# Performance work log

Hardware: AMD Instinct MI355X
Metric: run time of the kernel (lower is better)

## Reference

```python
import jax, jax.numpy as jnp
import numpy as np

B, T, D, H, O = 256, 512, 256, 512, 1


def setup_inputs() -> dict:
    key = jax.random.key(0)
    ks = jax.random.split(key, 7)
    s_ih = 1.0 / np.sqrt(H)
    return {
        "x": jax.random.normal(ks[0], (B, T, D), dtype=jnp.float32),
        "W_ih": jax.random.uniform(ks[1], (4 * H, D), jnp.float32, -s_ih, s_ih),
        "W_hh": jax.random.uniform(ks[2], (4 * H, H), jnp.float32, -s_ih, s_ih),
        "b_ih": jax.random.uniform(ks[3], (4 * H,), jnp.float32, -s_ih, s_ih),
        "b_hh": jax.random.uniform(ks[4], (4 * H,), jnp.float32, -s_ih, s_ih),
        "fc_w": jax.random.uniform(ks[5], (O, H), jnp.float32, -s_ih, s_ih),
        "fc_b": jax.random.uniform(ks[6], (O,), jnp.float32, -s_ih, s_ih),
    }


def reference(x, W_ih, W_hh, b_ih, b_hh, fc_w, fc_b):
    # x: [B, T, D]. Faithful to torch.nn.LSTMCell gate order (i, f, g, o).
    b = b_ih + b_hh
    # Precompute all input projections at once: [T, B, 4H]
    x_t = jnp.swapaxes(x, 0, 1)  # [T, B, D]
    x_proj = jnp.einsum("tbd,gd->tbg", x_t, W_ih) + b

    h0 = jnp.zeros((x.shape[0], W_hh.shape[1]), x.dtype)
    c0 = jnp.zeros_like(h0)

    def step(carry, xp):
        h, c = carry
        gates = xp + h @ W_hh.T  # [B, 4H]
        i, f, g, o = jnp.split(gates, 4, axis=-1)
        c_new = jax.nn.sigmoid(f) * c + jax.nn.sigmoid(i) * jnp.tanh(g)
        h_new = jax.nn.sigmoid(o) * jnp.tanh(c_new)
        return (h_new, c_new), None

    (h_last, _), _ = jax.lax.scan(step, (h0, c0), x_proj)
    out = h_last @ fc_w.T + fc_b  # [B, O]
    return jax.nn.sigmoid(out)
```

## Files before the change

### kernel.cpp

```cpp
#include <hip/hip_runtime.h>
#include <hip/hip_bf16.h>

#define BB 256
#define TT 512
#define DD 256
#define HH 512
#define G4H 2048
#define KTOT 768
#define APITCH 1552
#define WPITCH 1552

typedef unsigned short u16;
typedef unsigned int u32;
typedef __attribute__((ext_vector_type(8))) short bf16x8;
typedef __attribute__((ext_vector_type(4))) float f32x4;

__device__ __forceinline__ u16 f2bf(float f) {
  union { float f; unsigned u; } v; v.f = f;
  unsigned r = v.u + 0x7FFFu + ((v.u >> 16) & 1u);
  return (u16)(r >> 16);
}
__device__ __forceinline__ float bf2f(u16 b) {
  union { unsigned u; float f; } v; v.u = ((unsigned)b) << 16;
  return v.f;
}
__device__ __forceinline__ float fsigmoid(float x) { return 1.f / (1.f + __expf(-x)); }
__device__ __forceinline__ float ftanh(float x) { return 1.f - 2.f / (__expf(2.f * x) + 1.f); }

__device__ __forceinline__ bf16x8 ld16_sc(const u16* p) {
  bf16x8 r;
  asm volatile("global_load_dwordx4 %0, %1, off sc0 sc1" : "=v"(r) : "v"(p) : "memory");
  return r;
}
__device__ __forceinline__ void st4_sc(u16* p, u32 v) {
  asm volatile("global_store_dword %0, %1, off sc0 sc1" :: "v"(p), "v"(v) : "memory");
}
__device__ __forceinline__ void waitv0() {
  asm volatile("s_waitcnt vmcnt(0)" ::: "memory");
}

__global__ __launch_bounds__(256) void lstm_init(
    const float* __restrict__ W_ih, const float* __restrict__ W_hh,
    const float* __restrict__ b_ih, const float* __restrict__ b_hh,
    u16* __restrict__ Wc, float* __restrict__ bsum,
    u16* __restrict__ h0, u32* __restrict__ flags)
{
  int idx = blockIdx.x * 256 + threadIdx.x;
  if (idx < G4H * KTOT) {
    int r = idx / KTOT, k = idx - r * KTOT;
    float v = (k < HH) ? W_hh[r * HH + k] : W_ih[r * DD + (k - HH)];
    Wc[idx] = f2bf(v);
  }
  if (idx < G4H) bsum[idx] = b_ih[idx] + b_hh[idx];
  if (idx < BB * HH) h0[idx] = (u16)0;
  if (idx < 256) flags[idx] = 0u;
}

__global__ __launch_bounds__(256) void xconv(const float* __restrict__ x, u16* __restrict__ xbf)
{
  size_t i = ((size_t)blockIdx.x * 256 + threadIdx.x) * 8;
  float4 a = *(const float4*)(x + i);
  float4 b = *(const float4*)(x + i + 4);
  bf16x8 v;
  v[0] = (short)f2bf(a.x); v[1] = (short)f2bf(a.y);
  v[2] = (short)f2bf(a.z); v[3] = (short)f2bf(a.w);
  v[4] = (short)f2bf(b.x); v[5] = (short)f2bf(b.y);
  v[6] = (short)f2bf(b.z); v[7] = (short)f2bf(b.w);
  *(bf16x8*)(xbf + i) = v;
}

__global__ __launch_bounds__(256, 1) void lstm_persist(
    const u16* __restrict__ xbf, const u16* __restrict__ Wc,
    const float* __restrict__ bsum, u16* __restrict__ h_buf,
    u32* flags)
{
  __shared__ __align__(16) unsigned char Alds[32 * APITCH];
  __shared__ __align__(16) unsigned char Wlds[64 * WPITCH];
  __shared__ float g4[4][32][17];

  const int tid  = threadIdx.x;
  const int bg   = blockIdx.x & 7;
  const int sl   = blockIdx.x >> 3;
  const int lane = tid & 63;
  const int wv   = tid >> 6;
  const int lrow = lane & 15;
  const int lkb  = lane >> 4;

  #pragma unroll
  for (int j = 0; j < 24; ++j) {
    int c = tid + j * 256;
    int r = c / 96, col = c - r * 96;
    int q = r >> 4, u = r & 15;
    bf16x8 v = *(const bf16x8*)(Wc + (size_t)(q * HH + sl * 16 + u) * KTOT + col * 8);
    *(bf16x8*)(Wlds + r * WPITCH + col * 16) = v;
  }

  const int pb2 = tid >> 3;
  const int pu2 = (tid & 7) * 2;
  const int hu2 = sl * 16 + pu2;
  const int gb2 = bg * 32 + pb2;
  const float bi0 = bsum[hu2],          bi1 = bsum[hu2 + 1];
  const float bf0 = bsum[HH + hu2],     bf1 = bsum[HH + hu2 + 1];
  const float bg0 = bsum[2 * HH + hu2], bg1 = bsum[2 * HH + hu2 + 1];
  const float bo0 = bsum[3 * HH + hu2], bo1 = bsum[3 * HH + hu2 + 1];
  float c0 = 0.f, c1 = 0.f;
  u32* myflags = flags + bg * 32;

  for (int t = 0; t < TT; ++t) {
    const u16* __restrict__ h_in  = h_buf + (t & 1) * (BB * HH);
    u16* __restrict__ h_out = h_buf + ((t + 1) & 1) * (BB * HH);

    #pragma unroll
    for (int j = 0; j < 4; ++j) {
      int c = tid + j * 256;
      int row = c >> 5, col = c & 31;
      bf16x8 v = *(const bf16x8*)(xbf + ((size_t)(bg * 32 + row) * TT + t) * DD + col * 8);
      *(bf16x8*)(Alds + row * APITCH + 1024 + col * 16) = v;
    }
    if (t > 0 && wv == 0 && lane < 32) {
      while (__hip_atomic_load(&myflags[lane], __ATOMIC_RELAXED, __HIP_MEMORY_SCOPE_AGENT) < (u32)t)
        __builtin_amdgcn_s_sleep(1);
    }
    __syncthreads();

    bf16x8 hv[8];
    #pragma unroll
    for (int j = 0; j < 8; ++j) {
      int c = tid + j * 256;
      int row = c >> 6, col = c & 63;
      hv[j] = ld16_sc(h_in + (size_t)(bg * 32 + row) * HH + col * 8);
    }
    f32x4 acc0 = {0.f, 0.f, 0.f, 0.f};
    f32x4 acc1 = {0.f, 0.f, 0.f, 0.f};
    {
      const unsigned aox = (unsigned)(lrow * APITCH + 1024 + lkb * 16);
      const unsigned wox = (unsigned)((wv * 16 + lrow) * WPITCH + 1024 + lkb * 16);
      #pragma unroll
      for (int kc = 0; kc < 8; ++kc) {
        bf16x8 bfr = *(const bf16x8*)(Wlds + wox + kc * 64);
        bf16x8 a0  = *(const bf16x8*)(Alds + aox + kc * 64);
        bf16x8 a1  = *(const bf16x8*)(Alds + aox + 16u * APITCH + kc * 64);
        acc0 = __builtin_amdgcn_mfma_f32_16x16x32_bf16(a0, bfr, acc0, 0, 0, 0);
        acc1 = __builtin_amdgcn_mfma_f32_16x16x32_bf16(a1, bfr, acc1, 0, 0, 0);
      }
    }
    waitv0();
    __builtin_amdgcn_sched_barrier(0);
    #pragma unroll
    for (int j = 0; j < 8; ++j) {
      int c = tid + j * 256;
      int row = c >> 6, col = c & 63;
      *(bf16x8*)(Alds + row * APITCH + col * 16) = hv[j];
    }
    __syncthreads();

    {
      const unsigned ao = (unsigned)(lrow * APITCH + lkb * 16);
      const unsigned wo = (unsigned)((wv * 16 + lrow) * WPITCH + lkb * 16);
      #pragma unroll
      for (int kc = 0; kc < 16; ++kc) {
        bf16x8 bfr = *(const bf16x8*)(Wlds + wo + kc * 64);
        bf16x8 a0  = *(const bf16x8*)(Alds + ao + kc * 64);
        bf16x8 a1  = *(const bf16x8*)(Alds + ao + 16u * APITCH + kc * 64);
        acc0 = __builtin_amdgcn_mfma_f32_16x16x32_bf16(a0, bfr, acc0, 0, 0, 0);
        acc1 = __builtin_amdgcn_mfma_f32_16x16x32_bf16(a1, bfr, acc1, 0, 0, 0);
      }
    }
    #pragma unroll
    for (int r = 0; r < 4; ++r) {
      g4[wv][lkb * 4 + r][lrow]      = acc0[r];
      g4[wv][16 + lkb * 4 + r][lrow] = acc1[r];
    }
    __syncthreads();

    {
      float gi0 = g4[0][pb2][pu2]     + bi0, gi1 = g4[0][pb2][pu2 + 1] + bi1;
      float gf_0 = g4[1][pb2][pu2]    + bf0, gf_1 = g4[1][pb2][pu2 + 1] + bf1;
      float gg0 = g4[2][pb2][pu2]     + bg0, gg1 = g4[2][pb2][pu2 + 1] + bg1;
      float go0 = g4[3][pb2][pu2]     + bo0, go1 = g4[3][pb2][pu2 + 1] + bo1;
      c0 = fsigmoid(gf_0) * c0 + fsigmoid(gi0) * ftanh(gg0);
      c1 = fsigmoid(gf_1) * c1 + fsigmoid(gi1) * ftanh(gg1);
      u32 ha = (u32)f2bf(fsigmoid(go0) * ftanh(c0));
      u32 hb = (u32)f2bf(fsigmoid(go1) * ftanh(c1));
      st4_sc(h_out + (size_t)gb2 * HH + hu2, ha | (hb << 16));
    }
    waitv0();
    __syncthreads();
    if (tid == 0)
      __hip_atomic_store(&myflags[sl], (u32)(t + 1), __ATOMIC_RELAXED, __HIP_MEMORY_SCOPE_AGENT);
  }
}

__global__ __launch_bounds__(256) void lstm_final(
    const u16* __restrict__ h, const float* __restrict__ fc_w,
    const float* __restrict__ fc_b, float* __restrict__ out)
{
  int b = threadIdx.x;
  float s = 0.f;
  const u16* hp = h + (size_t)b * HH;
  #pragma unroll 8
  for (int k = 0; k < HH; k += 8) {
    bf16x8 v = *(const bf16x8*)(hp + k);
    #pragma unroll
    for (int j = 0; j < 8; ++j) s += bf2f((u16)v[j]) * fc_w[k + j];
  }
  s += fc_b[0];
  out[b] = fsigmoid(s);
}

extern "C" void kernel_launch(void* const* d_in, const int* in_sizes, int n_in,
                              void* d_out, int out_size, void* d_ws, size_t ws_size,
                              hipStream_t stream) {
  (void)in_sizes; (void)n_in; (void)out_size; (void)ws_size;
  const float* x    = (const float*)d_in[0];
  const float* W_ih = (const float*)d_in[1];
  const float* W_hh = (const float*)d_in[2];
  const float* b_ih = (const float*)d_in[3];
  const float* b_hh = (const float*)d_in[4];
  const float* fc_w = (const float*)d_in[5];
  const float* fc_b = (const float*)d_in[6];
  float* out = (float*)d_out;

  char* ws = (char*)d_ws;
  u16*   Wc    = (u16*)(ws);
  float* bsum  = (float*)(ws + 3145728);
  u16*   h_buf = (u16*)(ws + 3153920);
  u32*   flags = (u32*)(ws + 3678208);
  u16*   xbf   = (u16*)(ws + 4194304);

  lstm_init<<<6144, 256, 0, stream>>>(W_ih, W_hh, b_ih, b_hh, Wc, bsum, h_buf, flags);
  xconv<<<16384, 256, 0, stream>>>(x, xbf);
  void* args[] = { (void*)&xbf, (void*)&Wc, (void*)&bsum, (void*)&h_buf, (void*)&flags };
  (void)hipLaunchCooperativeKernel((void*)lstm_persist, dim3(256), dim3(256), args, 0, stream);
  lstm_final<<<1, 256, 0, stream>>>(h_buf, fc_w, fc_b, out);
}
```

Baseline: 1.689 ms.

## Hold LSTM weights in registers and use 32x32 MFMA with swizzled LDS

Each wave of the persistent LSTM kernel now keeps its slice of the combined weight matrix in VGPRs instead of LDS. It uses 32x32x16 MFMA with a split-K arrangement across wave pairs and two accumulators, plus an XOR-swizzled LDS layout for the activation tile. Weight rows are permuted at init to match the new tiling, and x is transposed to [T,B,D] so per-step loads are contiguous. The spin-wait sleep is removed. The aim is to cut per-step LDS traffic and latency on the serial recurrence, at the cost of heavy register pressure and an extra partial-sum reduction through shared memory.

```diff
diff --git a/kernel.cpp b/kernel.cpp
--- a/kernel.cpp
+++ b/kernel.cpp
@@ -7,13 +7,11 @@
 #define HH 512
 #define G4H 2048
 #define KTOT 768
-#define APITCH 1552
-#define WPITCH 1552
 
 typedef unsigned short u16;
 typedef unsigned int u32;
 typedef __attribute__((ext_vector_type(8))) short bf16x8;
-typedef __attribute__((ext_vector_type(4))) float f32x4;
+typedef __attribute__((ext_vector_type(16))) float f32x16;
 
 __device__ __forceinline__ u16 f2bf(float f) {
   union { float f; unsigned u; } v; v.f = f;
@@ -48,7 +46,11 @@
   int idx = blockIdx.x * 256 + threadIdx.x;
   if (idx < G4H * KTOT) {
     int r = idx / KTOT, k = idx - r * KTOT;
-    float v = (k < HH) ? W_hh[r * HH + k] : W_ih[r * DD + (k - HH)];
+    int slp = r >> 6, rem = r & 63;
+    int q = ((rem >> 5) << 1) | ((rem >> 4) & 1);
+    int u = rem & 15;
+    int srow = q * HH + slp * 16 + u;
+    float v = (k < HH) ? W_hh[srow * HH + k] : W_ih[srow * DD + (k - HH)];
     Wc[idx] = f2bf(v);
   }
   if (idx < G4H) bsum[idx] = b_ih[idx] + b_hh[idx];
@@ -56,43 +58,48 @@
   if (idx < 256) flags[idx] = 0u;
 }
 
-__global__ __launch_bounds__(256) void xconv(const float* __restrict__ x, u16* __restrict__ xbf)
-{
-  size_t i = ((size_t)blockIdx.x * 256 + threadIdx.x) * 8;
-  float4 a = *(const float4*)(x + i);
-  float4 b = *(const float4*)(x + i + 4);
+__global__ __launch_bounds__(256) void xconv(const float* __restrict__ x, u16* __restrict__ xbf2)
+{
+  size_t g = (size_t)blockIdx.x * 256 + threadIdx.x;
+  int d8 = (int)(g & 31);
+  int b  = (int)((g >> 5) & 255);
+  int t  = (int)(g >> 13);
+  const float* src = x + ((size_t)b * TT + t) * DD + d8 * 8;
+  float4 a = *(const float4*)(src);
+  float4 c = *(const float4*)(src + 4);
   bf16x8 v;
   v[0] = (short)f2bf(a.x); v[1] = (short)f2bf(a.y);
   v[2] = (short)f2bf(a.z); v[3] = (short)f2bf(a.w);
-  v[4] = (short)f2bf(b.x); v[5] = (short)f2bf(b.y);
-  v[6] = (short)f2bf(b.z); v[7] = (short)f2bf(b.w);
-  *(bf16x8*)(xbf + i) = v;
+  v[4] = (short)f2bf(c.x); v[5] = (short)f2bf(c.y);
+  v[6] = (short)f2bf(c.z); v[7] = (short)f2bf(c.w);
+  *(bf16x8*)(xbf2 + ((size_t)t * BB + b) * DD + d8 * 8) = v;
 }
 
 __global__ __launch_bounds__(256, 1) void lstm_persist(
-    const u16* __restrict__ xbf, const u16* __restrict__ Wc,
+    const u16* __restrict__ xbf2, const u16* __restrict__ Wc,
     const float* __restrict__ bsum, u16* __restrict__ h_buf,
     u32* flags)
 {
-  __shared__ __align__(16) unsigned char Alds[32 * APITCH];
-  __shared__ __align__(16) unsigned char Wlds[64 * WPITCH];
-  __shared__ float g4[4][32][17];
+  __shared__ __align__(16) unsigned char Alds[49152];
+  __shared__ float g4[2][2][32][66];
 
   const int tid  = threadIdx.x;
   const int bg   = blockIdx.x & 7;
   const int sl   = blockIdx.x >> 3;
   const int lane = tid & 63;
   const int wv   = tid >> 6;
-  const int lrow = lane & 15;
-  const int lkb  = lane >> 4;
-
-  #pragma unroll
-  for (int j = 0; j < 24; ++j) {
-    int c = tid + j * 256;
-    int r = c / 96, col = c - r * 96;
-    int q = r >> 4, u = r & 15;
-    bf16x8 v = *(const bf16x8*)(Wc + (size_t)(q * HH + sl * 16 + u) * KTOT + col * 8);
-    *(bf16x8*)(Wlds + r * WPITCH + col * 16) = v;
+  const int nb   = wv & 1;
+  const int kh   = wv >> 1;
+  const int l31  = lane & 31;
+  const int lhi  = lane >> 5;
+
+  bf16x8 wh[16], wx[8];
+  {
+    const u16* wb = Wc + (size_t)(sl * 64 + nb * 32 + l31) * KTOT + lhi * 8;
+    #pragma unroll
+    for (int i = 0; i < 16; ++i) wh[i] = *(const bf16x8*)(wb + kh * 256 + i * 16);
+    #pragma unroll
+    for (int i = 0; i < 8; ++i)  wx[i] = *(const bf16x8*)(wb + 512 + kh * 128 + i * 16);
   }
 
   const int pb2 = tid >> 3;
@@ -112,72 +119,69 @@
 
     #pragma unroll
     for (int j = 0; j < 4; ++j) {
-      int c = tid + j * 256;
-      int row = c >> 5, col = c & 31;
-      bf16x8 v = *(const bf16x8*)(xbf + ((size_t)(bg * 32 + row) * TT + t) * DD + col * 8);
-      *(bf16x8*)(Alds + row * APITCH + 1024 + col * 16) = v;
+      int idx = j * 256 + tid;
+      int row = idx & 31, d8 = idx >> 5;
+      bf16x8 v = *(const bf16x8*)(xbf2 + ((size_t)t * BB + bg * 32 + row) * DD + d8 * 8);
+      int kc = 32 + (d8 >> 1);
+      int slot = (((d8 & 1) << 5) | row) ^ ((kc & 15) << 2);
+      *(bf16x8*)(Alds + kc * 1024 + slot * 16) = v;
     }
     if (t > 0 && wv == 0 && lane < 32) {
-      while (__hip_atomic_load(&myflags[lane], __ATOMIC_RELAXED, __HIP_MEMORY_SCOPE_AGENT) < (u32)t)
-        __builtin_amdgcn_s_sleep(1);
+      while (__hip_atomic_load(&myflags[lane], __ATOMIC_RELAXED, __HIP_MEMORY_SCOPE_AGENT) < (u32)t) {}
     }
     __syncthreads();
 
     bf16x8 hv[8];
     #pragma unroll
     for (int j = 0; j < 8; ++j) {
-      int c = tid + j * 256;
-      int row = c >> 6, col = c & 63;
-      hv[j] = ld16_sc(h_in + (size_t)(bg * 32 + row) * HH + col * 8);
-    }
-    f32x4 acc0 = {0.f, 0.f, 0.f, 0.f};
-    f32x4 acc1 = {0.f, 0.f, 0.f, 0.f};
-    {
-      const unsigned aox = (unsigned)(lrow * APITCH + 1024 + lkb * 16);
-      const unsigned wox = (unsigned)((wv * 16 + lrow) * WPITCH + 1024 + lkb * 16);
-      #pragma unroll
-      for (int kc = 0; kc < 8; ++kc) {
-        bf16x8 bfr = *(const bf16x8*)(Wlds + wox + kc * 64);
-        bf16x8 a0  = *(const bf16x8*)(Alds + aox + kc * 64);
-        bf16x8 a1  = *(const bf16x8*)(Alds + aox + 16u * APITCH + kc * 64);
-        acc0 = __builtin_amdgcn_mfma_f32_16x16x32_bf16(a0, bfr, acc0, 0, 0, 0);
-        acc1 = __builtin_amdgcn_mfma_f32_16x16x32_bf16(a1, bfr, acc1, 0, 0, 0);
-      }
+      int idx = j * 256 + tid;
+      int row = idx & 31, col8 = idx >> 5;
+      hv[j] = ld16_sc(h_in + (size_t)(bg * 32 + row) * HH + col8 * 8);
+    }
+    f32x16 accA = {0,0,0,0,0,0,0,0,0,0,0,0,0,0,0,0};
+    f32x16 accB = {0,0,0,0,0,0,0,0,0,0,0,0,0,0,0,0};
+    #pragma unroll
+    for (int i = 0; i < 8; ++i) {
+      int kc = 32 + kh * 8 + i;
+      bf16x8 a = *(const bf16x8*)(Alds + kc * 1024 + (size_t)((lane ^ ((kc & 15) << 2)) * 16));
+      if (i & 1) accB = __builtin_amdgcn_mfma_f32_32x32x16_bf16(a, wx[i], accB, 0, 0, 0);
+      else       accA = __builtin_amdgcn_mfma_f32_32x32x16_bf16(a, wx[i], accA, 0, 0, 0);
     }
     waitv0();
     __builtin_amdgcn_sched_barrier(0);
     #pragma unroll
     for (int j = 0; j < 8; ++j) {
-      int c = tid + j * 256;
-      int row = c >> 6, col = c & 63;
-      *(bf16x8*)(Alds + row * APITCH + col * 16) = hv[j];
+      int idx = j * 256 + tid;
+      int row = idx & 31, col8 = idx >> 5;
+      int kc = col8 >> 1;
+      int slot = (((col8 & 1) << 5) | row) ^ ((kc & 15) << 2);
+      *(bf16x8*)(Alds + kc * 1024 + slot * 16) = hv[j];
+    }
+    __syncthreads();
+
+    #pragma unroll
+    for (int i = 0; i < 16; ++i) {
+      int kc = kh * 16 + i;
+      bf16x8 a = *(const bf16x8*)(Alds + kc * 1024 + (size_t)((lane ^ ((kc & 15) << 2)) * 16));
+      if (i & 1) accB = __builtin_amdgcn_mfma_f32_32x32x16_bf16(a, wh[i], accB, 0, 0, 0);
+      else       accA = __builtin_amdgcn_mfma_f32_32x32x16_bf16(a, wh[i], accA, 0, 0, 0);
+    }
+    #pragma unroll
+    for (int r = 0; r < 16; ++r) {
+      int grow = (r & 3) + 8 * (r >> 2) + 4 * lhi;
+      g4[kh][nb][grow][l31] = accA[r] + accB[r];
     }
     __syncthreads();
 
     {
-      const unsigned ao = (unsigned)(lrow * APITCH + lkb * 16);
-      const unsigned wo = (unsigned)((wv * 16 + lrow) * WPITCH + lkb * 16);
-      #pragma unroll
-      for (int kc = 0; kc < 16; ++kc) {
-        bf16x8 bfr = *(const bf16x8*)(Wlds + wo + kc * 64);
-        bf16x8 a0  = *(const bf16x8*)(Alds + ao + kc * 64);
-        bf16x8 a1  = *(const bf16x8*)(Alds + ao + 16u * APITCH + kc * 64);
-        acc0 = __builtin_amdgcn_mfma_f32_16x16x32_bf16(a0, bfr, acc0, 0, 0, 0);
-        acc1 = __builtin_amdgcn_mfma_f32_16x16x32_bf16(a1, bfr, acc1, 0, 0, 0);
-      }
-    }
-    #pragma unroll
-    for (int r = 0; r < 4; ++r) {
-      g4[wv][lkb * 4 + r][lrow]      = acc0[r];
-      g4[wv][16 + lkb * 4 + r][lrow] = acc1[r];
-    }
-    __syncthreads();
-
-    {
-      float gi0 = g4[0][pb2][pu2]     + bi0, gi1 = g4[0][pb2][pu2 + 1] + bi1;
-      float gf_0 = g4[1][pb2][pu2]    + bf0, gf_1 = g4[1][pb2][pu2 + 1] + bf1;
-      float gg0 = g4[2][pb2][pu2]     + bg0, gg1 = g4[2][pb2][pu2 + 1] + bg1;
-      float go0 = g4[3][pb2][pu2]     + bo0, go1 = g4[3][pb2][pu2 + 1] + bo1;
+      float gi0 = g4[0][0][pb2][pu2]      + g4[1][0][pb2][pu2]      + bi0;
+      float gf_0 = g4[0][0][pb2][16 + pu2] + g4[1][0][pb2][16 + pu2] + bf0;
+      float gg0 = g4[0][1][pb2][pu2]      + g4[1][1][pb2][pu2]      + bg0;
+      float go0 = g4[0][1][pb2][16 + pu2] + g4[1][1][pb2][16 + pu2] + bo0;
+      float gi1 = g4[0][0][pb2][pu2 + 1]      + g4[1][0][pb2][pu2 + 1]      + bi1;
+      float gf_1 = g4[0][0][pb2][17 + pu2] + g4[1][0][pb2][17 + pu2] + bf1;
+      float gg1 = g4[0][1][pb2][pu2 + 1]      + g4[1][1][pb2][pu2 + 1]      + bg1;
+      float go1 = g4[0][1][pb2][17 + pu2] + g4[1][1][pb2][17 + pu2] + bo1;
       c0 = fsigmoid(gf_0) * c0 + fsigmoid(gi0) * ftanh(gg0);
       c1 = fsigmoid(gf_1) * c1 + fsigmoid(gi1) * ftanh(gg1);
       u32 ha = (u32)f2bf(fsigmoid(go0) * ftanh(c0));
@@ -226,11 +230,11 @@
   float* bsum  = (float*)(ws + 3145728);
   u16*   h_buf = (u16*)(ws + 3153920);
   u32*   flags = (u32*)(ws + 3678208);
-  u16*   xbf   = (u16*)(ws + 4194304);
+  u16*   xbf2  = (u16*)(ws + 4194304);
 
   lstm_init<<<6144, 256, 0, stream>>>(W_ih, W_hh, b_ih, b_hh, Wc, bsum, h_buf, flags);
-  xconv<<<16384, 256, 0, stream>>>(x, xbf);
-  void* args[] = { (void*)&xbf, (void*)&Wc, (void*)&bsum, (void*)&h_buf, (void*)&flags };
+  xconv<<<16384, 256, 0, stream>>>(x, xbf2);
+  void* args[] = { (void*)&xbf2, (void*)&Wc, (void*)&bsum, (void*)&h_buf, (void*)&flags };
   (void)hipLaunchCooperativeKernel((void*)lstm_persist, dim3(256), dim3(256), args, 0, stream);
   lstm_final<<<1, 256, 0, stream>>>(h_buf, fc_w, fc_b, out);
 }
```

New measurement: 2.078 ms. 1.23x slower.

## Prefetch next-step x tile during current step and store x time-major

Applied to the files above, without the earlier changes.

The input conversion kernel now writes x in [T, B, D] order so each step's tile is contiguous. The persistent LSTM kernel loads the x tile for step t+1 into LDS at the end of step t, before the barrier and the flag wait, overlapping that latency with synchronization. The h-load index mapping is also reshuffled to be row-fastest. Correctness relies on the x LDS region being consumed before the prefetch write.

```diff
diff --git a/kernel.cpp b/kernel.cpp
--- a/kernel.cpp
+++ b/kernel.cpp
@@ -56,21 +56,25 @@
   if (idx < 256) flags[idx] = 0u;
 }
 
-__global__ __launch_bounds__(256) void xconv(const float* __restrict__ x, u16* __restrict__ xbf)
-{
-  size_t i = ((size_t)blockIdx.x * 256 + threadIdx.x) * 8;
-  float4 a = *(const float4*)(x + i);
-  float4 b = *(const float4*)(x + i + 4);
+__global__ __launch_bounds__(256) void xconv(const float* __restrict__ x, u16* __restrict__ xbf2)
+{
+  size_t g = (size_t)blockIdx.x * 256 + threadIdx.x;
+  int d8 = (int)(g & 31);
+  int b  = (int)((g >> 5) & 255);
+  int t  = (int)(g >> 13);
+  const float* src = x + ((size_t)b * TT + t) * DD + d8 * 8;
+  float4 a = *(const float4*)(src);
+  float4 c = *(const float4*)(src + 4);
   bf16x8 v;
   v[0] = (short)f2bf(a.x); v[1] = (short)f2bf(a.y);
   v[2] = (short)f2bf(a.z); v[3] = (short)f2bf(a.w);
-  v[4] = (short)f2bf(b.x); v[5] = (short)f2bf(b.y);
-  v[6] = (short)f2bf(b.z); v[7] = (short)f2bf(b.w);
-  *(bf16x8*)(xbf + i) = v;
+  v[4] = (short)f2bf(c.x); v[5] = (short)f2bf(c.y);
+  v[6] = (short)f2bf(c.z); v[7] = (short)f2bf(c.w);
+  *(bf16x8*)(xbf2 + ((size_t)t * BB + b) * DD + d8 * 8) = v;
 }
 
 __global__ __launch_bounds__(256, 1) void lstm_persist(
-    const u16* __restrict__ xbf, const u16* __restrict__ Wc,
+    const u16* __restrict__ xbf2, const u16* __restrict__ Wc,
     const float* __restrict__ bsum, u16* __restrict__ h_buf,
     u32* flags)
 {
@@ -106,17 +110,22 @@
   float c0 = 0.f, c1 = 0.f;
   u32* myflags = flags + bg * 32;
 
+  auto stage_x = [&](int tt) {
+    #pragma unroll
+    for (int j = 0; j < 4; ++j) {
+      int c = tid + j * 256;
+      int row = c >> 5, col = c & 31;
+      bf16x8 v = *(const bf16x8*)(xbf2 + ((size_t)tt * BB + bg * 32 + row) * DD + col * 8);
+      *(bf16x8*)(Alds + row * APITCH + 1024 + col * 16) = v;
+    }
+  };
+
+  stage_x(0);
+
   for (int t = 0; t < TT; ++t) {
     const u16* __restrict__ h_in  = h_buf + (t & 1) * (BB * HH);
     u16* __restrict__ h_out = h_buf + ((t + 1) & 1) * (BB * HH);
 
-    #pragma unroll
-    for (int j = 0; j < 4; ++j) {
-      int c = tid + j * 256;
-      int row = c >> 5, col = c & 31;
-      bf16x8 v = *(const bf16x8*)(xbf + ((size_t)(bg * 32 + row) * TT + t) * DD + col * 8);
-      *(bf16x8*)(Alds + row * APITCH + 1024 + col * 16) = v;
-    }
     if (t > 0 && wv == 0 && lane < 32) {
       while (__hip_atomic_load(&myflags[lane], __ATOMIC_RELAXED, __HIP_MEMORY_SCOPE_AGENT) < (u32)t)
         __builtin_amdgcn_s_sleep(1);
@@ -126,9 +135,9 @@
     bf16x8 hv[8];
     #pragma unroll
     for (int j = 0; j < 8; ++j) {
-      int c = tid + j * 256;
-      int row = c >> 6, col = c & 63;
-      hv[j] = ld16_sc(h_in + (size_t)(bg * 32 + row) * HH + col * 8);
+      int idx = j * 256 + tid;
+      int row = idx & 31, col8 = idx >> 5;
+      hv[j] = ld16_sc(h_in + (size_t)(bg * 32 + row) * HH + col8 * 8);
     }
     f32x4 acc0 = {0.f, 0.f, 0.f, 0.f};
     f32x4 acc1 = {0.f, 0.f, 0.f, 0.f};
@@ -148,9 +157,9 @@
     __builtin_amdgcn_sched_barrier(0);
     #pragma unroll
     for (int j = 0; j < 8; ++j) {
-      int c = tid + j * 256;
-      int row = c >> 6, col = c & 63;
-      *(bf16x8*)(Alds + row * APITCH + col * 16) = hv[j];
+      int idx = j * 256 + tid;
+      int row = idx & 31, col8 = idx >> 5;
+      *(bf16x8*)(Alds + row * APITCH + col8 * 16) = hv[j];
     }
     __syncthreads();
 
@@ -184,6 +193,7 @@
       u32 hb = (u32)f2bf(fsigmoid(go1) * ftanh(c1));
       st4_sc(h_out + (size_t)gb2 * HH + hu2, ha | (hb << 16));
     }
+    if (t + 1 < TT) stage_x(t + 1);
     waitv0();
     __syncthreads();
     if (tid == 0)
@@ -226,11 +236,11 @@
   float* bsum  = (float*)(ws + 3145728);
   u16*   h_buf = (u16*)(ws + 3153920);
   u32*   flags = (u32*)(ws + 3678208);
-  u16*   xbf   = (u16*)(ws + 4194304);
+  u16*   xbf2  = (u16*)(ws + 4194304);
 
   lstm_init<<<6144, 256, 0, stream>>>(W_ih, W_hh, b_ih, b_hh, Wc, bsum, h_buf, flags);
-  xconv<<<16384, 256, 0, stream>>>(x, xbf);
-  void* args[] = { (void*)&xbf, (void*)&Wc, (void*)&bsum, (void*)&h_buf, (void*)&flags };
+  xconv<<<16384, 256, 0, stream>>>(x, xbf2);
+  void* args[] = { (void*)&xbf2, (void*)&Wc, (void*)&bsum, (void*)&h_buf, (void*)&flags };
   (void)hipLaunchCooperativeKernel((void*)lstm_persist, dim3(256), dim3(256), args, 0, stream);
   lstm_final<<<1, 256, 0, stream>>>(h_buf, fc_w, fc_b, out);
 }
```

Result: slower. 2.285 ms (+35.2%).
